# Performance work log

Measured on AMD Instinct MI355X. Metric: run time of the kernel, lower is better.

The kernel has to match this reference:

```python
import jax, jax.numpy as jnp
import numpy as np

N = 50000       # nodes
E = 800000      # edges (avg degree 16)
F_IN = 128      # in_feats
H = 128         # h_feats
C = 16          # num_classes
EPS = 1e-5      # BatchNorm eps


def setup_inputs() -> dict:
    key = jax.random.key(0)
    ks = jax.random.split(key, 26)
    rn = lambda k, shape: jax.random.normal(k, shape, dtype=jnp.float32) * 0.05
    zeros = lambda d: jnp.zeros((d,), jnp.float32)
    ones = lambda d: jnp.ones((d,), jnp.float32)
    return {
        "features": jax.random.normal(ks[0], (N, F_IN), dtype=jnp.float32),
        "src": jax.random.randint(ks[1], (E,), 0, N),
        "dst": jax.random.randint(ks[2], (E,), 0, N),
        # input_encoder
        "W_in": rn(ks[3], (F_IN, H)), "b_in": zeros(H),
        # SAGEConv layer 0: H -> 2H (fc_self, fc_neigh, bias)
        "Ws0": rn(ks[4], (H, 2 * H)), "Wn0": rn(ks[5], (H, 2 * H)), "bs0": zeros(2 * H),
        # BatchNorm1d(2H) eval-mode stats
        "g0": ones(2 * H), "bt0": zeros(2 * H),
        "m0": rn(ks[6], (2 * H,)),
        "v0": jax.random.uniform(ks[7], (2 * H,), jnp.float32, 0.5, 1.5),
        # SAGEConv layer 1: 2H -> H
        "Ws1": rn(ks[8], (2 * H, H)), "Wn1": rn(ks[9], (2 * H, H)), "bs1": zeros(H),
        # BatchNorm1d(H)
        "g1": ones(H), "bt1": zeros(H),
        "m1": rn(ks[10], (H,)),
        "v1": jax.random.uniform(ks[11], (H,), jnp.float32, 0.5, 1.5),
        # relation_encoder: 2H -> H
        "Wr": rn(ks[12], (2 * H, H)), "br": zeros(H),
        # classifier: H -> H//2 -> C
        "Wc1": rn(ks[13], (H, H // 2)), "bc1": zeros(H // 2),
        "Wc2": rn(ks[14], (H // 2, C)), "bc2": zeros(C),
    }


def _bn(x, g, b, m, v):
    # eval-mode BatchNorm1d with running stats
    return (x - m) * jax.lax.rsqrt(v + EPS) * g + b


def _sage(h, src, dst, Ws, Wn, b, inv_deg):
    # DGL SAGEConv 'mean': out = fc_self(h_dst) + fc_neigh(mean_{u in N(v)} h_u) + bias
    neigh = jax.ops.segment_sum(h[src], dst, num_segments=N) * inv_deg  # [N, d_in]
    return h @ Ws + neigh @ Wn + b


def reference(features, src, dst, W_in, b_in, Ws0, Wn0, bs0, g0, bt0, m0, v0,
              Ws1, Wn1, bs1, g1, bt1, m1, v1, Wr, br, Wc1, bc1, Wc2, bc2):
    deg = jax.ops.segment_sum(jnp.ones((E,), jnp.float32), dst, num_segments=N)
    inv_deg = (1.0 / jnp.maximum(deg, 1.0))[:, None]  # [N, 1]

    h0 = jax.nn.relu(features @ W_in + b_in)                       # [N, H]
    h = jax.nn.relu(_bn(_sage(h0, src, dst, Ws0, Wn0, bs0, inv_deg), g0, bt0, m0, v0))  # [N, 2H]
    h = jax.nn.relu(_bn(_sage(h, src, dst, Ws1, Wn1, bs1, inv_deg), g1, bt1, m1, v1))   # [N, H]

    h_final = jax.nn.relu(jnp.concatenate([h0, h], axis=1) @ Wr + br)  # [N, H]
    return jax.nn.relu(h_final @ Wc1 + bc1) @ Wc2 + bc2                # [N, C]
```

## Files before the change

### kernel.cpp

```cpp
#include <hip/hip_runtime.h>

typedef short v8s __attribute__((ext_vector_type(8)));
typedef float v4f __attribute__((ext_vector_type(4)));
typedef unsigned short u16;
typedef unsigned int u32;

#define NNODES 50000
#define NEDGES 800000
#define CSTRIDE 64

#define NB 512
#define BSPAN 98
#define EBLK 98
#define NBU 511
#define SUBCAP 48

__device__ __forceinline__ float bf2f(u16 b) {
    u32 u = ((u32)b) << 16;
    return __builtin_bit_cast(float, u);
}
__device__ __forceinline__ u16 f2bf(float f) {
    u32 u = __builtin_bit_cast(u32, f);
    u32 r = (u + 0x7fffu + ((u >> 16) & 1u)) >> 16;
    return (u16)r;
}

struct PackDesc { const float* B1; const float* B2; int K1, K2, N, csplit, start; u16* out; };
struct PackArgs { PackDesc d[6]; int total; };

__global__ __launch_bounds__(256) void prep_pack(
    PackArgs pa,
    const float* b_in, const float* bs0, const float* g0, const float* bt0,
    const float* m0, const float* v0,
    const float* bs1, const float* g1, const float* bt1, const float* m1, const float* v1,
    const float* br, const float* bc1, const float* bc2,
    float* sc_in, float* sh_in, float* sc0, float* sh0, float* sc1, float* sh1,
    float* sc_r, float* sh_r, float* sh_c1, float* sh_c2) {
    int t = threadIdx.x;
    if (blockIdx.x == 0) {
        if (t < 128) { sc_in[t] = 1.f; sh_in[t] = b_in[t]; }
        if (t < 256) {
            float s = g0[t] * rsqrtf(v0[t] + 1e-5f);
            sc0[t] = s;
            sh0[t] = (bs0[t] - m0[t]) * s + bt0[t];
        }
        if (t < 128) {
            float s = g1[t] * rsqrtf(v1[t] + 1e-5f);
            sc1[t] = s;
            sh1[t] = (bs1[t] - m1[t]) * s + bt1[t];
        }
        if (t < 128) { sc_r[t] = 1.f; sh_r[t] = br[t]; }
        if (t < 64)  { sh_c1[t] = bc1[t]; }
        if (t < 16)  { sh_c2[t] = bc2[t]; }
    }
    int tid = blockIdx.x * 256 + t;
    if (tid >= pa.total) return;
    int s = 0;
    for (int i = 1; i < 6; i++)
        if (tid >= pa.d[i].start) s = i;
    const PackDesc& D = pa.d[s];
    int tt = tid - D.start;
    int frag = tt >> 9;
    int rem = tt & 511;
    int lane = rem >> 3;
    int j = rem & 7;
    int nf = D.N >> 4;
    int kt = frag / nf, nt = frag - kt * nf;
    int k = kt * 32 + (lane >> 4) * 8 + j;
    int n = nt * 16 + (lane & 15);
    float v;
    if (D.csplit)
        v = (n < D.csplit) ? D.B1[(size_t)k * D.csplit + n]
                           : D.B2[(size_t)k * (D.N - D.csplit) + (n - D.csplit)];
    else
        v = (k < D.K1) ? D.B1[(size_t)k * D.N + n]
                       : D.B2[(size_t)(k - D.K1) * D.N + n];
    D.out[tt] = f2bf(v);
}

template <int BN, int CW, int KT, int KSPLIT, bool RELU, bool F32OUT, bool AF32>
__device__ __forceinline__ void gemm_body(
    int bx,
    const void* __restrict__ A0v, int lda0,
    const void* __restrict__ A1v, int lda1,
    int M,
    const v8s* __restrict__ Bp,
    const float* __restrict__ scale, const float* __restrict__ shift,
    u16* __restrict__ C, float* __restrict__ Cf, int ldc) {
    constexpr int NFW = BN / 16 / CW;
    constexpr int RW = 4 / CW;
    int lane = threadIdx.x & 63;
    int wave = threadIdx.x >> 6;
    int colw = wave % CW;
    int roww = wave / CW;
    int quad = lane >> 4;
    int l16 = lane & 15;
    int base = bx * (64 * RW) + roww * 64;

    v4f acc[4][NFW];
#pragma unroll
    for (int rg = 0; rg < 4; rg++)
#pragma unroll
        for (int nt = 0; nt < NFW; nt++) acc[rg][nt] = (v4f)0.0f;

    size_t o0[4], o1[4];
#pragma unroll
    for (int rg = 0; rg < 4; rg++) {
        int r = base + rg * 16 + l16;
        if (r > M - 1) r = M - 1;
        o0[rg] = (size_t)r * lda0 + quad * 8;
        o1[rg] = (size_t)r * lda1 + quad * 8;
    }

    auto load_a = [&](const void* Av, size_t off) -> v8s {
        if constexpr (AF32) {
            const float* p = (const float*)Av + off;
            float4 x = *(const float4*)p;
            float4 y = *(const float4*)(p + 4);
            v8s a;
            a[0] = (short)f2bf(x.x); a[1] = (short)f2bf(x.y);
            a[2] = (short)f2bf(x.z); a[3] = (short)f2bf(x.w);
            a[4] = (short)f2bf(y.x); a[5] = (short)f2bf(y.y);
            a[6] = (short)f2bf(y.z); a[7] = (short)f2bf(y.w);
            return a;
        } else {
            return *(const v8s*)((const u16*)Av + off);
        }
    };

#pragma unroll
    for (int kt = 0; kt < KT; kt++) {
        v8s a[4];
#pragma unroll
        for (int rg = 0; rg < 4; rg++) {
            if (kt < KSPLIT) a[rg] = load_a(A0v, o0[rg] + kt * 32);
            else             a[rg] = load_a(A1v, o1[rg] + (size_t)(kt - KSPLIT) * 32);
        }
        const v8s* bb = Bp + (size_t)kt * (BN / 16) * 64 + (colw * NFW) * 64 + lane;
#pragma unroll
        for (int nt = 0; nt < NFW; nt++) {
            v8s b = bb[nt * 64];
#pragma unroll
            for (int rg = 0; rg < 4; rg++)
                acc[rg][nt] = __builtin_amdgcn_mfma_f32_16x16x32_bf16(a[rg], b, acc[rg][nt], 0, 0, 0);
        }
    }

    int colbase = colw * (NFW * 16);
#pragma unroll
    for (int rg = 0; rg < 4; rg++) {
        int rbase = base + rg * 16 + quad * 4;
#pragma unroll
        for (int nt = 0; nt < NFW; nt++) {
            int col = colbase + nt * 16 + l16;
            float s = scale[col], sh = shift[col];
#pragma unroll
            for (int i = 0; i < 4; i++) {
                int row = rbase + i;
                if (row < M) {
                    float v = acc[rg][nt][i] * s + sh;
                    if (RELU) v = v > 0.f ? v : 0.f;
                    if (F32OUT) Cf[(size_t)row * ldc + col] = v;
                    else C[(size_t)row * ldc + col] = f2bf(v);
                }
            }
        }
    }
}

__device__ __forceinline__ u32 gather_mean2(
    const u16* __restrict__ nl, int d, const u16* __restrict__ Hl, int ldh) {
    float a0 = 0.f, a1 = 0.f, b0 = 0.f, b1 = 0.f;
    float c0 = 0.f, c1 = 0.f, d0 = 0.f, d1 = 0.f;
    float e0 = 0.f, e1 = 0.f, f0 = 0.f, f1 = 0.f;
    float g0 = 0.f, g1 = 0.f, h0_ = 0.f, h1_ = 0.f;
    int e = 0;
    for (; e + 8 <= d; e += 8) {
        int u0 = nl[e], u1 = nl[e + 1], u2 = nl[e + 2], u3 = nl[e + 3];
        int u4 = nl[e + 4], u5 = nl[e + 5], u6 = nl[e + 6], u7 = nl[e + 7];
        u32 w0 = *(const u32*)(Hl + (size_t)u0 * ldh);
        u32 w1 = *(const u32*)(Hl + (size_t)u1 * ldh);
        u32 w2 = *(const u32*)(Hl + (size_t)u2 * ldh);
        u32 w3 = *(const u32*)(Hl + (size_t)u3 * ldh);
        u32 w4 = *(const u32*)(Hl + (size_t)u4 * ldh);
        u32 w5 = *(const u32*)(Hl + (size_t)u5 * ldh);
        u32 w6 = *(const u32*)(Hl + (size_t)u6 * ldh);
        u32 w7 = *(const u32*)(Hl + (size_t)u7 * ldh);
        a0 += bf2f((u16)w0); a1 += bf2f((u16)(w0 >> 16));
        b0 += bf2f((u16)w1); b1 += bf2f((u16)(w1 >> 16));
        c0 += bf2f((u16)w2); c1 += bf2f((u16)(w2 >> 16));
        d0 += bf2f((u16)w3); d1 += bf2f((u16)(w3 >> 16));
        e0 += bf2f((u16)w4); e1 += bf2f((u16)(w4 >> 16));
        f0 += bf2f((u16)w5); f1 += bf2f((u16)(w5 >> 16));
        g0 += bf2f((u16)w6); g1 += bf2f((u16)(w6 >> 16));
        h0_ += bf2f((u16)w7); h1_ += bf2f((u16)(w7 >> 16));
    }
    for (; e + 4 <= d; e += 4) {
        int u0 = nl[e], u1 = nl[e + 1], u2 = nl[e + 2], u3 = nl[e + 3];
        u32 w0 = *(const u32*)(Hl + (size_t)u0 * ldh);
        u32 w1 = *(const u32*)(Hl + (size_t)u1 * ldh);
        u32 w2 = *(const u32*)(Hl + (size_t)u2 * ldh);
        u32 w3 = *(const u32*)(Hl + (size_t)u3 * ldh);
        a0 += bf2f((u16)w0); a1 += bf2f((u16)(w0 >> 16));
        b0 += bf2f((u16)w1); b1 += bf2f((u16)(w1 >> 16));
        c0 += bf2f((u16)w2); c1 += bf2f((u16)(w2 >> 16));
        d0 += bf2f((u16)w3); d1 += bf2f((u16)(w3 >> 16));
    }
    for (; e < d; e++) {
        int u = nl[e];
        u32 w = *(const u32*)(Hl + (size_t)u * ldh);
        a0 += bf2f((u16)w); a1 += bf2f((u16)(w >> 16));
    }
    float s = 1.0f / (float)(d > 0 ? d : 1);
    float r0 = ((a0 + b0) + (c0 + d0)) + ((e0 + f0) + (g0 + h0_));
    float r1 = ((a1 + b1) + (c1 + d1)) + ((e1 + f1) + (g1 + h1_));
    return (u32)f2bf(r0 * s) | ((u32)f2bf(r1 * s) << 16);
}

__global__ __launch_bounds__(256) void mega_binA_h0(
    const int* __restrict__ src, const int* __restrict__ dst,
    int* __restrict__ gcnt, u32* __restrict__ gbuf,
    const float* __restrict__ features,
    const v8s* __restrict__ Winp,
    const float* __restrict__ sc_in, const float* __restrict__ sh_in,
    u16* __restrict__ hcat0) {
    int bx = blockIdx.x;
    if (bx < EBLK) {
        __shared__ int lcnt[NB];
        int t = threadIdx.x;
        for (int i = t; i < NB; i += 256) lcnt[i] = 0;
        __syncthreads();
        int ebase = bx * 8192;
#pragma unroll
        for (int c = 0; c < 8; c++) {
            int e0 = ebase + c * 1024 + t * 4;
            if (e0 + 4 <= NEDGES) {
                int4 s4 = *(const int4*)(src + e0);
                int4 d4 = *(const int4*)(dst + e0);
                int ss[4] = {s4.x, s4.y, s4.z, s4.w};
                int dd[4] = {d4.x, d4.y, d4.z, d4.w};
#pragma unroll
                for (int j = 0; j < 4; j++) {
                    int b = dd[j] / BSPAN;
                    int dl = dd[j] - b * BSPAN;
                    int p = atomicAdd(&lcnt[b], 1);
                    if (p < SUBCAP)
                        gbuf[((size_t)b * EBLK + bx) * SUBCAP + p] =
                            ((u32)dl << 16) | (u32)ss[j];
                }
            } else {
#pragma unroll
                for (int j = 0; j < 4; j++) {
                    int e = e0 + j;
                    if (e < NEDGES) {
                        int d = dst[e];
                        int b = d / BSPAN;
                        int dl = d - b * BSPAN;
                        int p = atomicAdd(&lcnt[b], 1);
                        if (p < SUBCAP)
                            gbuf[((size_t)b * EBLK + bx) * SUBCAP + p] =
                                ((u32)dl << 16) | (u32)src[e];
                    }
                }
            }
        }
        __syncthreads();
        for (int i = t; i < NB; i += 256) {
            int c = lcnt[i];
            if (c > SUBCAP) c = SUBCAP;
            gcnt[bx * NB + i] = c;
        }
    } else {
        gemm_body<128, 4, 4, 4, true, false, true>(
            bx - EBLK, features, 128, features, 128, NNODES,
            Winp, sc_in, sh_in, hcat0, nullptr, 256);
    }
}

__global__ __launch_bounds__(1024) void fill_bg(
    const u32* __restrict__ gbuf, const int* __restrict__ gcnt,
    u16* __restrict__ csr, int* __restrict__ cursor,
    const u16* __restrict__ H, u16* __restrict__ D) {
    __shared__ u16 lcsr[BSPAN * CSTRIDE];
    __shared__ int lcur[BSPAN];
    __shared__ int scnt[EBLK];
    int b = blockIdx.x;
    int t = threadIdx.x;
    int v0 = b * BSPAN;
    int span = NNODES - v0;
    if (span > BSPAN) span = BSPAN;
    for (int i = t; i < BSPAN; i += 1024) lcur[i] = 0;
    for (int i = t; i < EBLK; i += 1024) scnt[i] = gcnt[i * NB + b];
    __syncthreads();
    const u32* gb = gbuf + (size_t)b * EBLK * SUBCAP;
    for (int s = t; s < EBLK * SUBCAP; s += 1024) {
        int blk = s / SUBCAP;
        int idx = s - blk * SUBCAP;
        if (idx < scnt[blk]) {
            u32 pk = gb[s];
            int dl = pk >> 16;
            int p = atomicAdd(&lcur[dl], 1);
            if (p < CSTRIDE) lcsr[(dl << 6) + p] = (u16)(pk & 0xffffu);
        }
    }
    __syncthreads();
    {
        const u32* lw = (const u32*)lcsr;
        u32* gw = (u32*)(csr + ((size_t)v0 << 6));
        int nw = span * (CSTRIDE / 2);
        for (int i = t; i < nw; i += 1024) gw[i] = lw[i];
        for (int i = t; i < span; i += 1024) cursor[v0 + i] = lcur[i];
    }
    int lane = t & 63;
    int wv = t >> 6;
    for (int i = wv; i < span; i += 16) {
        int d = lcur[i];
        if (d > CSTRIDE) d = CSTRIDE;
        u32 o = gather_mean2(&lcsr[i << 6], d, H + lane * 2, 256);
        *(u32*)(D + (size_t)(v0 + i) * 256 + lane * 2) = o;
    }
}

__global__ __launch_bounds__(512) void gemm_h1ps(
    const u16* __restrict__ A,
    const v8s* __restrict__ B0,
    const float* __restrict__ sc0, const float* __restrict__ sh0,
    const v8s* __restrict__ B1,
    u16* __restrict__ ps, int M) {
    constexpr int LSTR = 264;
    __shared__ u16 at[64 * LSTR];
    __shared__ u16 h1s[64 * LSTR];
    int t = threadIdx.x;
    int lane = t & 63;
    int wave = t >> 6;
    int quad = lane >> 4;
    int l16 = lane & 15;
    int base = blockIdx.x * 64;

#pragma unroll
    for (int k = 0; k < 4; k++) {
        int cid = t + k * 512;
        int row = cid >> 5;
        int seg = cid & 31;
        int r = base + row;
        if (r > M - 1) r = M - 1;
        v8s v = *(const v8s*)(A + (size_t)r * 256 + seg * 8);
        *(v8s*)(&at[row * LSTR + seg * 8]) = v;
    }
    __syncthreads();

    v4f acc[4][2];
#pragma unroll
    for (int rg = 0; rg < 4; rg++)
#pragma unroll
        for (int nt = 0; nt < 2; nt++) acc[rg][nt] = (v4f)0.0f;

#pragma unroll
    for (int kt = 0; kt < 8; kt++) {
        v8s a[4];
#pragma unroll
        for (int rg = 0; rg < 4; rg++)
            a[rg] = *(const v8s*)(&at[(rg * 16 + l16) * LSTR + quad * 8 + kt * 32]);
        const v8s* bb = B0 + (size_t)kt * 16 * 64 + (wave * 2) * 64 + lane;
#pragma unroll
        for (int nt = 0; nt < 2; nt++) {
            v8s b = bb[nt * 64];
#pragma unroll
            for (int rg = 0; rg < 4; rg++)
                acc[rg][nt] = __builtin_amdgcn_mfma_f32_16x16x32_bf16(a[rg], b, acc[rg][nt], 0, 0, 0);
        }
    }
    int colbase = wave * 32;
#pragma unroll
    for (int rg = 0; rg < 4; rg++) {
        int rowL = rg * 16 + quad * 4;
#pragma unroll
        for (int nt = 0; nt < 2; nt++) {
            int col = colbase + nt * 16 + l16;
            float s = sc0[col], sh = sh0[col];
#pragma unroll
            for (int i = 0; i < 4; i++) {
                float v = acc[rg][nt][i] * s + sh;
                v = v > 0.f ? v : 0.f;
                h1s[(rowL + i) * LSTR + col] = f2bf(v);
            }
        }
    }
    __syncthreads();

#pragma unroll
    for (int rg = 0; rg < 4; rg++)
#pragma unroll
        for (int nt = 0; nt < 2; nt++) acc[rg][nt] = (v4f)0.0f;
#pragma unroll
    for (int kt = 0; kt < 8; kt++) {
        v8s a[4];
#pragma unroll
        for (int rg = 0; rg < 4; rg++)
            a[rg] = *(const v8s*)(&h1s[(rg * 16 + l16) * LSTR + quad * 8 + kt * 32]);
        const v8s* bb = B1 + (size_t)kt * 16 * 64 + (wave * 2) * 64 + lane;
#pragma unroll
        for (int nt = 0; nt < 2; nt++) {
            v8s b = bb[nt * 64];
#pragma unroll
            for (int rg = 0; rg < 4; rg++)
                acc[rg][nt] = __builtin_amdgcn_mfma_f32_16x16x32_bf16(a[rg], b, acc[rg][nt], 0, 0, 0);
        }
    }
    __syncthreads();
#pragma unroll
    for (int rg = 0; rg < 4; rg++) {
        int rowL = rg * 16 + quad * 4;
#pragma unroll
        for (int nt = 0; nt < 2; nt++) {
            int col = colbase + nt * 16 + l16;
#pragma unroll
            for (int i = 0; i < 4; i++)
                at[(rowL + i) * LSTR + col] = f2bf(acc[rg][nt][i]);
        }
    }
    __syncthreads();

#pragma unroll
    for (int k = 0; k < 4; k++) {
        int cid = t + k * 512;
        int row = cid >> 5;
        int seg = cid & 31;
        int r = base + row;
        if (r < M) {
            v8s v = *(const v8s*)(&at[row * LSTR + seg * 8]);
            *(v8s*)(ps + (size_t)r * 256 + seg * 8) = v;
        }
    }
}

__global__ __launch_bounds__(256) void agg_h2(
    const int* __restrict__ cursor, const u16* __restrict__ csr,
    const u16* __restrict__ ps,
    const float* __restrict__ sc1, const float* __restrict__ sh1,
    u16* __restrict__ h2, int n) {
    int v = blockIdx.x * 4 + (threadIdx.x >> 6);
    if (v >= n) return;
    int lane = threadIdx.x & 63;
    int d = cursor[v];
    if (d > CSTRIDE) d = CSTRIDE;
    u32 sv = *(const u32*)(ps + (size_t)v * 256 + lane * 2);
    u32 nm = gather_mean2(csr + ((size_t)v << 6), d, ps + 128 + lane * 2, 256);
    int col = lane * 2;
    float x0 = (bf2f((u16)sv) + bf2f((u16)nm)) * sc1[col] + sh1[col];
    float x1 = (bf2f((u16)(sv >> 16)) + bf2f((u16)(nm >> 16))) * sc1[col + 1] + sh1[col + 1];
    x0 = x0 > 0.f ? x0 : 0.f;
    x1 = x1 > 0.f ? x1 : 0.f;
    u32 o = (u32)f2bf(x0) | ((u32)f2bf(x1) << 16);
    *(u32*)(h2 + (size_t)v * 128 + lane * 2) = o;
}

__global__ __launch_bounds__(256) void gemm_chain(
    const u16* __restrict__ hcat0,
    const u16* __restrict__ h2,
    const v8s* __restrict__ Wrp, const float* __restrict__ sc_r, const float* __restrict__ sh_r,
    const v8s* __restrict__ Wm1p, const float* __restrict__ sh_c1,
    const v8s* __restrict__ Wm2p, const float* __restrict__ sh_c2,
    float* __restrict__ out, int M) {
    constexpr int LS = 136;
    __shared__ u16 tile[64 * LS];
    int lane = threadIdx.x & 63;
    int wv = threadIdx.x >> 6;
    int quad = lane >> 4;
    int l16 = lane & 15;
    int base = blockIdx.x * 64;

    v4f acc[4][2];
#pragma unroll
    for (int rg = 0; rg < 4; rg++)
#pragma unroll
        for (int nt = 0; nt < 2; nt++) acc[rg][nt] = (v4f)0.0f;
    size_t o0[4], o1[4];
#pragma unroll
    for (int rg = 0; rg < 4; rg++) {
        int r = base + rg * 16 + l16;
        if (r > M - 1) r = M - 1;
        o0[rg] = (size_t)r * 256 + quad * 8;
        o1[rg] = (size_t)r * 128 + quad * 8;
    }
#pragma unroll
    for (int kt = 0; kt < 8; kt++) {
        v8s a[4];
#pragma unroll
        for (int rg = 0; rg < 4; rg++) {
            if (kt < 4) a[rg] = *(const v8s*)(hcat0 + o0[rg] + kt * 32);
            else        a[rg] = *(const v8s*)(h2 + o1[rg] + (size_t)(kt - 4) * 32);
        }
        const v8s* bb = Wrp + (size_t)kt * 8 * 64 + (wv * 2) * 64 + lane;
#pragma unroll
        for (int nt = 0; nt < 2; nt++) {
            v8s b = bb[nt * 64];
#pragma unroll
            for (int rg = 0; rg < 4; rg++)
                acc[rg][nt] = __builtin_amdgcn_mfma_f32_16x16x32_bf16(a[rg], b, acc[rg][nt], 0, 0, 0);
        }
    }
    {
        int colbase = wv * 32;
#pragma unroll
        for (int rg = 0; rg < 4; rg++) {
            int rowL = rg * 16 + quad * 4;
#pragma unroll
            for (int nt = 0; nt < 2; nt++) {
                int col = colbase + nt * 16 + l16;
                float s = sc_r[col], sh = sh_r[col];
#pragma unroll
                for (int i = 0; i < 4; i++) {
                    float v = acc[rg][nt][i] * s + sh;
                    v = v > 0.f ? v : 0.f;
                    tile[(rowL + i) * LS + col] = f2bf(v);
                }
            }
        }
    }
    __syncthreads();

    v4f a2[4];
#pragma unroll
    for (int rg = 0; rg < 4; rg++) a2[rg] = (v4f)0.0f;
#pragma unroll
    for (int kt = 0; kt < 4; kt++) {
        v8s a[4];
#pragma unroll
        for (int rg = 0; rg < 4; rg++)
            a[rg] = *(const v8s*)(&tile[(rg * 16 + l16) * LS + quad * 8 + kt * 32]);
        v8s b = Wm1p[(size_t)kt * 4 * 64 + wv * 64 + lane];
#pragma unroll
        for (int rg = 0; rg < 4; rg++)
            a2[rg] = __builtin_amdgcn_mfma_f32_16x16x32_bf16(a[rg], b, a2[rg], 0, 0, 0);
    }
    __syncthreads();
    {
        int col = wv * 16 + l16;
        float sh = sh_c1[col];
#pragma unroll
        for (int rg = 0; rg < 4; rg++) {
            int rowL = rg * 16 + quad * 4;
#pragma unroll
            for (int i = 0; i < 4; i++) {
                float v = a2[rg][i] + sh;
                v = v > 0.f ? v : 0.f;
                tile[(rowL + i) * LS + col] = f2bf(v);
            }
        }
    }
    __syncthreads();

    v4f a3 = (v4f)0.0f;
#pragma unroll
    for (int kt = 0; kt < 2; kt++) {
        v8s a = *(const v8s*)(&tile[(wv * 16 + l16) * LS + quad * 8 + kt * 32]);
        v8s b = Wm2p[kt * 64 + lane];
        a3 = __builtin_amdgcn_mfma_f32_16x16x32_bf16(a, b, a3, 0, 0, 0);
    }
    int row = base + wv * 16 + quad * 4;
    float sh = sh_c2[l16];
#pragma unroll
    for (int i = 0; i < 4; i++) {
        int r = row + i;
        if (r < M) out[(size_t)r * 16 + l16] = a3[i] + sh;
    }
}

extern "C" void kernel_launch(void* const* d_in, const int* in_sizes, int n_in,
                              void* d_out, int out_size, void* d_ws, size_t ws_size,
                              hipStream_t stream) {
    const int N = NNODES;
    const float* features = (const float*)d_in[0];
    const int* src = (const int*)d_in[1];
    const int* dst = (const int*)d_in[2];
    float* out = (float*)d_out;

    char* w = (char*)d_ws;
    auto alloc = [&](size_t bytes) -> char* {
        char* p = w;
        w += (bytes + 255) & ~(size_t)255;
        return p;
    };
    int*   cursor = (int*)alloc((size_t)N * 4);
    u16*   csr    = (u16*)alloc((size_t)N * CSTRIDE * 2);
    u16*   hcat0  = (u16*)alloc((size_t)N * 256 * 2);
    u16*   ps     = (u16*)alloc((size_t)N * 256 * 2);
    u16*   h2     = (u16*)alloc((size_t)N * 128 * 2);
    u32*   gbuf   = (u32*)alloc((size_t)NBU * EBLK * SUBCAP * 4);
    int*   gcnt   = (int*)alloc((size_t)EBLK * NB * 4);
    u16*   Winp   = (u16*)alloc(128 * 128 * 2);
    u16*   Wc0p   = (u16*)alloc(256 * 256 * 2);
    u16*   Wsn1p  = (u16*)alloc(256 * 256 * 2);
    u16*   Wrp    = (u16*)alloc(256 * 128 * 2);
    u16*   Wm1p   = (u16*)alloc(128 * 64 * 2);
    u16*   Wm2p   = (u16*)alloc(64 * 16 * 2);
    float* sc_in = (float*)alloc(128 * 4); float* sh_in = (float*)alloc(128 * 4);
    float* sc0   = (float*)alloc(256 * 4); float* sh0   = (float*)alloc(256 * 4);
    float* sc1   = (float*)alloc(128 * 4); float* sh1   = (float*)alloc(128 * 4);
    float* sc_r  = (float*)alloc(128 * 4); float* sh_r  = (float*)alloc(128 * 4);
    float* sh_c1 = (float*)alloc(64 * 4);
    float* sh_c2 = (float*)alloc(16 * 4);

    PackArgs pa;
    int st = 0;
    auto seg = [&](int i, const float* B1, const float* B2, int K1, int K2,
                   int Nn, int csp, u16* o) {
        pa.d[i] = {B1, B2, K1, K2, Nn, csp, st, o};
        st += (K1 + K2) * Nn;
    };
    seg(0, (const float*)d_in[3], nullptr, 128, 0, 128, 0, Winp);
    seg(1, (const float*)d_in[5], (const float*)d_in[6], 128, 128, 256, 0, Wc0p);
    seg(2, (const float*)d_in[12], (const float*)d_in[13], 256, 0, 256, 128, Wsn1p);
    seg(3, (const float*)d_in[19], nullptr, 256, 0, 128, 0, Wrp);
    seg(4, (const float*)d_in[21], nullptr, 128, 0, 64, 0, Wm1p);
    seg(5, (const float*)d_in[23], nullptr, 64, 0, 16, 0, Wm2p);
    pa.total = st;

    prep_pack<<<(st + 255) / 256, 256, 0, stream>>>(
        pa,
        (const float*)d_in[4], (const float*)d_in[7], (const float*)d_in[8],
        (const float*)d_in[9], (const float*)d_in[10], (const float*)d_in[11],
        (const float*)d_in[14], (const float*)d_in[15], (const float*)d_in[16],
        (const float*)d_in[17], (const float*)d_in[18], (const float*)d_in[20],
        (const float*)d_in[22], (const float*)d_in[24],
        sc_in, sh_in, sc0, sh0, sc1, sh1, sc_r, sh_r, sh_c1, sh_c2);

    int gb64 = (N + 63) / 64;
    mega_binA_h0<<<EBLK + gb64, 256, 0, stream>>>(
        src, dst, gcnt, gbuf, features, (const v8s*)Winp, sc_in, sh_in, hcat0);
    fill_bg<<<NBU, 1024, 0, stream>>>(gbuf, gcnt, csr, cursor, hcat0, hcat0 + 128);
    gemm_h1ps<<<gb64, 512, 0, stream>>>(hcat0, (const v8s*)Wc0p, sc0, sh0,
                                        (const v8s*)Wsn1p, ps, N);
    agg_h2<<<(N + 3) / 4, 256, 0, stream>>>(cursor, csr, ps, sc1, sh1, h2, N);
    gemm_chain<<<gb64, 256, 0, stream>>>(
        hcat0, h2, (const v8s*)Wrp, sc_r, sh_r,
        (const v8s*)Wm1p, sh_c1, (const v8s*)Wm2p, sh_c2, out, N);
}
```

Before: 242.9 us.

## Stage gemm_chain A-tile in LDS with coalesced loads and use 8 waves

```diff
diff --git a/kernel.cpp b/kernel.cpp
--- a/kernel.cpp
+++ b/kernel.cpp
@@ -455,115 +455,111 @@
     *(u32*)(h2 + (size_t)v * 128 + lane * 2) = o;
 }
 
-__global__ __launch_bounds__(256) void gemm_chain(
+__global__ __launch_bounds__(512) void gemm_chain(
     const u16* __restrict__ hcat0,
     const u16* __restrict__ h2,
     const v8s* __restrict__ Wrp, const float* __restrict__ sc_r, const float* __restrict__ sh_r,
     const v8s* __restrict__ Wm1p, const float* __restrict__ sh_c1,
     const v8s* __restrict__ Wm2p, const float* __restrict__ sh_c2,
     float* __restrict__ out, int M) {
-    constexpr int LS = 136;
-    __shared__ u16 tile[64 * LS];
-    int lane = threadIdx.x & 63;
-    int wv = threadIdx.x >> 6;
+    constexpr int LSTR = 264;
+    __shared__ u16 at[64 * LSTR];
+    int t = threadIdx.x;
+    int lane = t & 63;
+    int wv = t >> 6;
     int quad = lane >> 4;
     int l16 = lane & 15;
     int base = blockIdx.x * 64;
 
-    v4f acc[4][2];
-#pragma unroll
-    for (int rg = 0; rg < 4; rg++)
-#pragma unroll
-        for (int nt = 0; nt < 2; nt++) acc[rg][nt] = (v4f)0.0f;
-    size_t o0[4], o1[4];
-#pragma unroll
-    for (int rg = 0; rg < 4; rg++) {
-        int r = base + rg * 16 + l16;
+#pragma unroll
+    for (int k = 0; k < 4; k++) {
+        int cid = t + k * 512;
+        int row = cid >> 5;
+        int seg = cid & 31;
+        int r = base + row;
         if (r > M - 1) r = M - 1;
-        o0[rg] = (size_t)r * 256 + quad * 8;
-        o1[rg] = (size_t)r * 128 + quad * 8;
-    }
+        v8s v;
+        if (seg < 16) v = *(const v8s*)(hcat0 + (size_t)r * 256 + seg * 8);
+        else          v = *(const v8s*)(h2 + (size_t)r * 128 + (seg - 16) * 8);
+        *(v8s*)(&at[row * LSTR + seg * 8]) = v;
+    }
+    __syncthreads();
+
+    v4f acc[4];
+#pragma unroll
+    for (int rg = 0; rg < 4; rg++) acc[rg] = (v4f)0.0f;
 #pragma unroll
     for (int kt = 0; kt < 8; kt++) {
-        v8s a[4];
+        v8s b = Wrp[(size_t)kt * 8 * 64 + wv * 64 + lane];
 #pragma unroll
         for (int rg = 0; rg < 4; rg++) {
-            if (kt < 4) a[rg] = *(const v8s*)(hcat0 + o0[rg] + kt * 32);
-            else        a[rg] = *(const v8s*)(h2 + o1[rg] + (size_t)(kt - 4) * 32);
-        }
-        const v8s* bb = Wrp + (size_t)kt * 8 * 64 + (wv * 2) * 64 + lane;
-#pragma unroll
-        for (int nt = 0; nt < 2; nt++) {
-            v8s b = bb[nt * 64];
-#pragma unroll
-            for (int rg = 0; rg < 4; rg++)
-                acc[rg][nt] = __builtin_amdgcn_mfma_f32_16x16x32_bf16(a[rg], b, acc[rg][nt], 0, 0, 0);
-        }
-    }
+            v8s a = *(const v8s*)(&at[(rg * 16 + l16) * LSTR + quad * 8 + kt * 32]);
+            acc[rg] = __builtin_amdgcn_mfma_f32_16x16x32_bf16(a, b, acc[rg], 0, 0, 0);
+        }
+    }
+    __syncthreads();
     {
-        int colbase = wv * 32;
+        int col = wv * 16 + l16;
+        float s = sc_r[col], sh = sh_r[col];
 #pragma unroll
         for (int rg = 0; rg < 4; rg++) {
             int rowL = rg * 16 + quad * 4;
 #pragma unroll
-            for (int nt = 0; nt < 2; nt++) {
-                int col = colbase + nt * 16 + l16;
-                float s = sc_r[col], sh = sh_r[col];
-#pragma unroll
-                for (int i = 0; i < 4; i++) {
-                    float v = acc[rg][nt][i] * s + sh;
-                    v = v > 0.f ? v : 0.f;
-                    tile[(rowL + i) * LS + col] = f2bf(v);
-                }
+            for (int i = 0; i < 4; i++) {
+                float v = acc[rg][i] * s + sh;
+                v = v > 0.f ? v : 0.f;
+                at[(rowL + i) * LSTR + col] = f2bf(v);
             }
         }
     }
     __syncthreads();
 
-    v4f a2[4];
-#pragma unroll
-    for (int rg = 0; rg < 4; rg++) a2[rg] = (v4f)0.0f;
+    int roww = wv >> 2;
+    int colw = wv & 3;
+    v4f a2[2];
+#pragma unroll
+    for (int rg = 0; rg < 2; rg++) a2[rg] = (v4f)0.0f;
 #pragma unroll
     for (int kt = 0; kt < 4; kt++) {
-        v8s a[4];
-#pragma unroll
-        for (int rg = 0; rg < 4; rg++)
-            a[rg] = *(const v8s*)(&tile[(rg * 16 + l16) * LS + quad * 8 + kt * 32]);
-        v8s b = Wm1p[(size_t)kt * 4 * 64 + wv * 64 + lane];
-#pragma unroll
-        for (int rg = 0; rg < 4; rg++)
-            a2[rg] = __builtin_amdgcn_mfma_f32_16x16x32_bf16(a[rg], b, a2[rg], 0, 0, 0);
+        v8s b = Wm1p[(size_t)kt * 4 * 64 + colw * 64 + lane];
+#pragma unroll
+        for (int rg = 0; rg < 2; rg++) {
+            v8s a = *(const v8s*)(&at[(roww * 32 + rg * 16 + l16) * LSTR + quad * 8 + kt * 32]);
+            a2[rg] = __builtin_amdgcn_mfma_f32_16x16x32_bf16(a, b, a2[rg], 0, 0, 0);
+        }
     }
     __syncthreads();
     {
-        int col = wv * 16 + l16;
+        int col = colw * 16 + l16;
         float sh = sh_c1[col];
 #pragma unroll
-        for (int rg = 0; rg < 4; rg++) {
-            int rowL = rg * 16 + quad * 4;
+        for (int rg = 0; rg < 2; rg++) {
+            int rowL = roww * 32 + rg * 16 + quad * 4;
 #pragma unroll
             for (int i = 0; i < 4; i++) {
                 float v = a2[rg][i] + sh;
                 v = v > 0.f ? v : 0.f;
-                tile[(rowL + i) * LS + col] = f2bf(v);
+                at[(rowL + i) * LSTR + col] = f2bf(v);
             }
         }
     }
     __syncthreads();
 
-    v4f a3 = (v4f)0.0f;
-#pragma unroll
-    for (int kt = 0; kt < 2; kt++) {
-        v8s a = *(const v8s*)(&tile[(wv * 16 + l16) * LS + quad * 8 + kt * 32]);
-        v8s b = Wm2p[kt * 64 + lane];
-        a3 = __builtin_amdgcn_mfma_f32_16x16x32_bf16(a, b, a3, 0, 0, 0);
-    }
-    int row = base + wv * 16 + quad * 4;
-    float sh = sh_c2[l16];
-#pragma unroll
-    for (int i = 0; i < 4; i++) {
-        int r = row + i;
-        if (r < M) out[(size_t)r * 16 + l16] = a3[i] + sh;
+    if (wv < 4) {
+        v4f a3 = (v4f)0.0f;
+#pragma unroll
+        for (int kt = 0; kt < 2; kt++) {
+            v8s a = *(const v8s*)(&at[(wv * 16 + l16) * LSTR + quad * 8 + kt * 32]);
+            v8s b = Wm2p[kt * 64 + lane];
+            a3 = __builtin_amdgcn_mfma_f32_16x16x32_bf16(a, b, a3, 0, 0, 0);
+        }
+        int row = base + wv * 16 + quad * 4;
+        float sh = sh_c2[l16];
+#pragma unroll
+        for (int i = 0; i < 4; i++) {
+            int r = row + i;
+            if (r < M) out[(size_t)r * 16 + l16] = a3[i] + sh;
+        }
     }
 }
 
@@ -633,7 +629,7 @@
     gemm_h1ps<<<gb64, 512, 0, stream>>>(hcat0, (const v8s*)Wc0p, sc0, sh0,
                                         (const v8s*)Wsn1p, ps, N);
     agg_h2<<<(N + 3) / 4, 256, 0, stream>>>(cursor, csr, ps, sc1, sh1, h2, N);
-    gemm_chain<<<gb64, 256, 0, stream>>>(
+    gemm_chain<<<gb64, 512, 0, stream>>>(
         hcat0, h2, (const v8s*)Wrp, sc_r, sh_r,
         (const v8s*)Wm1p, sh_c1, (const v8s*)Wm2p, sh_c2, out, N);
 }
```

Measured after the change: 234.9 us. 3.3% less time.
